# Performance work log

Measured on AMD Instinct MI355X. Metric: run time of the kernel, lower is better.

The kernel has to match this reference:

```python
import jax, jax.numpy as jnp
import numpy as np

L, H, DH = 2, 4, 64
D = H * DH                      # hidden_dim*heads = 256
B = 8                           # graphs per batch
NI_PG, ND_PG = 1024, 512        # inst/data nodes per graph
NI, ND = B * NI_PG, B * ND_PG
NPG = NI_PG + ND_PG
KPOOL = NPG // 2                # SAGPooling ratio=0.5
EC, EI, EO, EK = 65536, 32768, 32768, 8192


def setup_inputs():
    key = jax.random.key(0)
    ks = iter(jax.random.split(key, 64))
    def edges(ns, nd, e):
        k1, k2 = jax.random.split(next(ks))
        return jnp.stack([jax.random.randint(k1, (e,), 0, ns),
                          jax.random.randint(k2, (e,), 0, nd)]).astype(jnp.int32)
    inp = {}
    for g in ('g1', 'g2'):
        inp[g + '_x_inst'] = 0.1 * jax.random.normal(next(ks), (NI, D), jnp.float32)
        inp[g + '_x_data'] = 0.1 * jax.random.normal(next(ks), (ND, D), jnp.float32)
        inp[g + '_e_control'] = edges(NI, NI, EC)
        inp[g + '_e_input'] = edges(ND, NI, EI)
        inp[g + '_e_output'] = edges(NI, ND, EO)
        inp[g + '_e_call'] = edges(NI, NI, EK)
    s = 1.0 / np.sqrt(D)
    def w(*shape):
        return s * jax.random.normal(next(ks), shape, jnp.float32)
    for name in ('hgt_Wk', 'hgt_Wq', 'hgt_Wv', 'hgt_Wo'):
        inp[name] = w(L, 2, 2, D, D)   # [layer, direction, node_type, D, D]
    sh = 1.0 / np.sqrt(DH)
    inp['hgt_arel'] = sh * jax.random.normal(next(ks), (L, 2, 4, H, DH, DH), jnp.float32)
    inp['hgt_mrel'] = sh * jax.random.normal(next(ks), (L, 2, 4, H, DH, DH), jnp.float32)
    inp['hgt_prel'] = jnp.ones((L, 2, 4, H), jnp.float32)
    inp['hgt_skip'] = jnp.ones((L, 2, 2), jnp.float32)
    inp['pool_W'] = w(D, 1)
    inp['pool_att'] = 0.1 * jax.random.normal(next(ks), (2,), jnp.float32)
    inp['pool_bias'] = jnp.zeros((1,), jnp.float32)
    for name in ('trans_Wq', 'trans_Wk', 'trans_Wv', 'trans_Wo'):
        inp[name] = w(D, D)
    inp['trans_ln_g'] = jnp.ones((D,), jnp.float32)
    inp['trans_ln_b'] = jnp.zeros((D,), jnp.float32)
    return inp


def _seg_softmax_agg(scores, vals, col, n):
    # scores [E,H], vals [E,H,DH], softmax over incoming edges per dst node
    m = jax.ops.segment_max(scores, col, num_segments=n)
    a = jnp.exp(scores - m[col])
    den = jax.ops.segment_sum(a, col, num_segments=n)
    alpha = a / (den[col] + 1e-16)
    return jax.ops.segment_sum(alpha[..., None] * vals, col, num_segments=n)


def _hgt_conv(xs, rels, Wk, Wq, Wv, Wo, arel, mrel, prel, skip):
    # xs: [x_inst, x_data]; rels: list of (rel_idx, src_t, dst_t, row, col)
    ns = [x.shape[0] for x in xs]
    K = [(x @ Wk[t]).reshape(-1, H, DH) for t, x in enumerate(xs)]
    Q = [(x @ Wq[t]).reshape(-1, H, DH) for t, x in enumerate(xs)]
    V = [(x @ Wv[t]).reshape(-1, H, DH) for t, x in enumerate(xs)]
    buf = {0: ([], [], []), 1: ([], [], [])}
    for r, st, dt, row, col in rels:
        ke = jnp.einsum('ehd,hdf->ehf', K[st][row], arel[r])
        ve = jnp.einsum('ehd,hdf->ehf', V[st][row], mrel[r])
        sc = (Q[dt][col] * ke).sum(-1) * prel[r] / np.sqrt(DH)   # [E,H]
        buf[dt][0].append(sc); buf[dt][1].append(ve); buf[dt][2].append(col)
    out = []
    for t, x in enumerate(xs):
        sc = jnp.concatenate(buf[t][0])
        ve = jnp.concatenate(buf[t][1])
        col = jnp.concatenate(buf[t][2])
        agg = _seg_softmax_agg(sc, ve, col, ns[t]).reshape(ns[t], D)
        o = jax.nn.gelu(agg, approximate=False) @ Wo[t]
        g = jax.nn.sigmoid(skip[t])
        out.append(g * o + (1.0 - g) * x)
    return out


def _dir_hgt(xs, E, P, l):
    (rc, cc), (ri, ci), (ro, co), (rk, ck) = [(e[0], e[1]) for e in E]
    fwd_rels = [(0, 0, 0, rc, cc), (1, 1, 0, ri, ci), (2, 0, 1, ro, co), (3, 0, 0, rk, ck)]
    rev_rels = [(0, 0, 0, cc, rc), (1, 0, 1, ci, ri), (2, 1, 0, co, ro), (3, 0, 0, ck, rk)]
    of = _hgt_conv(xs, fwd_rels, *[p[l, 0] for p in P])
    orv = _hgt_conv(xs, rev_rels, *[p[l, 1] for p in P])
    return [0.5 * a + 0.5 * b for a, b in zip(of, orv)]   # alpha = 0.5


def _branch(x_i, x_d, ec, ei, eo, ek, P, pool_W, pool_att, pool_bias, tq, tk, tv, to, lg, lb):
    xs = [x_i, x_d]
    E = (ec, ei, eo, ek)
    for l in range(L):
        xs = _dir_hgt(xs, E, P, l)
        xs = [jax.nn.relu(x) for x in xs]        # dropout is identity at eval
    x = jnp.concatenate(xs, 0)                   # to_homogeneous: inst then data
    N = NI + ND
    loops = jnp.arange(N, dtype=jnp.int32)       # GATConv add_self_loops=True
    row = jnp.concatenate([ec[0], ei[0] + NI, eo[0], ek[0], loops])
    col = jnp.concatenate([ec[1], ei[1], eo[1] + NI, ek[1], loops])
    # SAGPooling score via 1-channel GATConv
    h = x @ pool_W                               # [N,1]
    e = jax.nn.leaky_relu(pool_att[0] * h[row, 0] + pool_att[1] * h[col, 0], negative_slope=0.2)
    m = jax.ops.segment_max(e, col, num_segments=N)
    a = jnp.exp(e - m[col])
    den = jax.ops.segment_sum(a, col, num_segments=N)
    score = jax.ops.segment_sum((a / (den[col] + 1e-16)) * h[row, 0], col, num_segments=N) + pool_bias[0]
    # regroup nodes per graph (graphs contiguous within each node type block)
    sg = jnp.concatenate([score[:NI].reshape(B, NI_PG), score[NI:].reshape(B, ND_PG)], 1)
    xg = jnp.concatenate([x[:NI].reshape(B, NI_PG, D), x[NI:].reshape(B, ND_PG, D)], 1)
    vals, idx = jax.lax.top_k(sg, KPOOL)
    xp = jnp.take_along_axis(xg, idx[:, :, None], axis=1) * jnp.tanh(vals)[:, :, None]
    # global transformer attention over pooled nodes of each graph (TransConv)
    q = (xp @ tq).reshape(B, KPOOL, H, DH)
    k_ = (xp @ tk).reshape(B, KPOOL, H, DH)
    v = (xp @ tv).reshape(B, KPOOL, H, DH)
    att = jax.nn.softmax(jnp.einsum('bqhd,bkhd->bhqk', q, k_) / np.sqrt(DH), -1)
    o = jnp.einsum('bhqk,bkhd->bqhd', att, v).reshape(B, KPOOL, D) @ to
    y = xp + o
    mu = y.mean(-1, keepdims=True)
    var = ((y - mu) ** 2).mean(-1, keepdims=True)
    gatt = lg * (y - mu) / jnp.sqrt(var + 1e-5) + lb
    feat = jnp.concatenate([xp, gatt], -1)       # [B, KPOOL, 2D]
    return feat.sum(1)                           # global_add_pool -> [B, 2D]


def reference(g1_x_inst, g1_x_data, g1_e_control, g1_e_input, g1_e_output, g1_e_call,
              g2_x_inst, g2_x_data, g2_e_control, g2_e_input, g2_e_output, g2_e_call,
              hgt_Wk, hgt_Wq, hgt_Wv, hgt_Wo, hgt_arel, hgt_mrel, hgt_prel, hgt_skip,
              pool_W, pool_att, pool_bias,
              trans_Wq, trans_Wk, trans_Wv, trans_Wo, trans_ln_g, trans_ln_b):
    P = (hgt_Wk, hgt_Wq, hgt_Wv, hgt_Wo, hgt_arel, hgt_mrel, hgt_prel, hgt_skip)
    u = _branch(g1_x_inst, g1_x_data, g1_e_control, g1_e_input, g1_e_output, g1_e_call,
                P, pool_W, pool_att, pool_bias, trans_Wq, trans_Wk, trans_Wv, trans_Wo,
                trans_ln_g, trans_ln_b)
    v = _branch(g2_x_inst, g2_x_data, g2_e_control, g2_e_input, g2_e_output, g2_e_call,
                P, pool_W, pool_att, pool_bias, trans_Wq, trans_Wk, trans_Wv, trans_Wo,
                trans_ln_g, trans_ln_b)
    num = (u * v).sum(-1)
    den = jnp.maximum(jnp.linalg.norm(u, axis=-1), 1e-8) * jnp.maximum(jnp.linalg.norm(v, axis=-1), 1e-8)
    return num / den                             # cosine similarity, [B]
```

## Files before the change

### kernel.cpp

```cpp
#include <hip/hip_runtime.h>
#include <math.h>
#include <stdint.h>

#define LL 2
#define HH 4
#define DHH 64
#define DD 256
#define BB 8
#define NI 8192
#define ND 4096
#define NROW 12288
#define KPOOL 768
#define EC 65536
#define EI 32768
#define EO 32768
#define EK 8192
#define EHGT (EC+EI+EO+EK)

typedef unsigned short u16;
typedef short bf16x8 __attribute__((ext_vector_type(8)));
typedef float f32x4 __attribute__((ext_vector_type(4)));
typedef unsigned short u16x4 __attribute__((ext_vector_type(4)));

__device__ inline float gelu_f(float x){ return 0.5f*x*(1.f+erff(x*0.70710678118654752f)); }
__device__ inline u16 f2b(float x){ uint32_t u=__float_as_uint(x); return (u16)((u + 0x7fffu + ((u>>16)&1u))>>16); }
__device__ inline float b2f(u16 h){ return __uint_as_float(((uint32_t)h)<<16); }

__global__ void fill_u32(uint32_t* p, uint32_t v, int n){
    int i = blockIdx.x*256 + threadIdx.x;
    if(i<n) p[i]=v;
}

__global__ void cvt_split(const float* __restrict__ A, int nA, const float* __restrict__ B, int nB,
                          u16* __restrict__ oh, u16* __restrict__ ol){
    int i = (blockIdx.x*256 + threadIdx.x)*4;
    int tot = nA + nB;
    if(i >= tot) return;
    float4 v = (i < nA) ? *(const float4*)(A + i) : *(const float4*)(B + (i - nA));
    float vv[4] = {v.x, v.y, v.z, v.w};
    u16x4 h4, l4;
    #pragma unroll
    for(int j=0;j<4;j++){
        float x = vv[j];
        u16 h = f2b(x);
        h4[j] = h;
        l4[j] = f2b(x - b2f(h));
    }
    *(u16x4*)(oh + i) = h4;
    *(u16x4*)(ol + i) = l4;
}

struct WCArgs { const float* in[8]; u16* oh[8]; u16* ol[8]; int cnt[8]; int nr; };
__global__ void wcvt_split(WCArgs a){
    int mat = blockIdx.y, ri = 0;
    while(ri < a.nr-1 && mat >= a.cnt[ri]){ mat -= a.cnt[ri]; ri++; }
    const float* in = a.in[ri] + (size_t)mat*65536;
    u16* oh = a.oh[ri] + (size_t)mat*65536;
    u16* ol = a.ol[ri] + (size_t)mat*65536;
    int n = blockIdx.x, k = threadIdx.x;
    float x = in[(size_t)k*DD + n];
    u16 h = f2b(x);
    oh[n*DD + k] = h;
    ol[n*DD + k] = f2b(x - b2f(h));
}

__global__ void wcvt_wo(const float* __restrict__ Wo, const float* __restrict__ skip,
                        u16* __restrict__ oh, u16* __restrict__ ol){
    int combo = blockIdx.y;
    int l = combo >> 1, t = combo & 1;
    int n = blockIdx.x, k = threadIdx.x;
    #pragma unroll
    for(int dir=0;dir<2;dir++){
        int wi = (l*2+dir)*2 + t;
        float gg = 1.f/(1.f+expf(-skip[wi]));
        float x = 0.5f*gg*Wo[(size_t)wi*65536 + (size_t)k*DD + n];
        size_t o = (size_t)combo*131072 + (size_t)n*512 + dir*256 + k;
        u16 hh = f2b(x);
        oh[o] = hh;
        ol[o] = f2b(x - b2f(hh));
    }
}

struct GDesc { const u16* Ah; const u16* Al; const u16* Bh; const u16* Bl;
               float* C; u16* Oh; u16* Ol;
               const float* X; const float* skipp;
               int mblks; int mode; int prec; int kdim; };
struct GArgs { GDesc d[20]; int nd; };

__global__ __launch_bounds__(256) void gemm_mfma(GArgs ga){
    __shared__ u16 SBUF[2*128*64];
    char* Abuf = (char*)SBUF;
    char* Bbuf = (char*)(SBUF + 128*64);
    int mb = blockIdx.x, di = 0;
    while(di < ga.nd-1 && mb >= ga.d[di].mblks){ mb -= ga.d[di].mblks; di++; }
    GDesc g = ga.d[di];
    const int prec = g.prec;
    const int KD = g.kdim;
    const int m0 = mb*128, n0 = blockIdx.y*128;
    const int tid = threadIdx.x;
    const int lane = tid & 63, wid = tid >> 6;
    const int wm = (wid>>1)*64, wn = (wid&1)*64;
    const int l15 = lane & 15, l4 = lane >> 4;
    const int srow = tid >> 1, hf = tid & 1;
    const int ssw = (srow&7)<<4;
    const int c0 = (hf*32) ^ ssw;
    const int c1 = (hf*32+16) ^ ssw;
    const int c2 = (64+hf*32) ^ ssw;
    const int c3 = (64+hf*32+16) ^ ssw;
    const int rbyte = srow*128;
    const u16* __restrict__ Aph = g.Ah + (size_t)(m0 + srow)*KD + hf*16;
    const u16* __restrict__ Apl = g.Al + (size_t)(m0 + srow)*KD + hf*16;
    const u16* __restrict__ Bph = g.Bh + (size_t)(n0 + srow)*KD + hf*16;
    const u16* __restrict__ Bpl = g.Bl + (size_t)(n0 + srow)*KD + hf*16;
    f32x4 acc[4][4] = {};
    bf16x8 r0, r1, r2, r3, r4, r5, r6, r7;
    r0 = *(const bf16x8*)(Aph);
    r1 = *(const bf16x8*)(Aph + 8);
    r4 = *(const bf16x8*)(Bph);
    r5 = *(const bf16x8*)(Bph + 8);
    if(!prec){
        r2 = *(const bf16x8*)(Apl);
        r3 = *(const bf16x8*)(Apl + 8);
        r6 = *(const bf16x8*)(Bpl);
        r7 = *(const bf16x8*)(Bpl + 8);
    }
    for(int k0=0;k0<KD;k0+=32){
        __syncthreads();
        *(bf16x8*)(Abuf + rbyte + c0) = r0; *(bf16x8*)(Abuf + rbyte + c1) = r1;
        *(bf16x8*)(Bbuf + rbyte + c0) = r4; *(bf16x8*)(Bbuf + rbyte + c1) = r5;
        if(!prec){
            *(bf16x8*)(Abuf + rbyte + c2) = r2; *(bf16x8*)(Abuf + rbyte + c3) = r3;
            *(bf16x8*)(Bbuf + rbyte + c2) = r6; *(bf16x8*)(Bbuf + rbyte + c3) = r7;
        }
        __syncthreads();
        if(k0 + 32 < KD){
            int kn = k0 + 32;
            r0 = *(const bf16x8*)(Aph + kn);     r1 = *(const bf16x8*)(Aph + kn + 8);
            r4 = *(const bf16x8*)(Bph + kn);     r5 = *(const bf16x8*)(Bph + kn + 8);
            if(!prec){
                r2 = *(const bf16x8*)(Apl + kn); r3 = *(const bf16x8*)(Apl + kn + 8);
                r6 = *(const bf16x8*)(Bpl + kn); r7 = *(const bf16x8*)(Bpl + kn + 8);
            }
        }
        bf16x8 afh[4], bfh[4];
        #pragma unroll
        for(int i=0;i<4;i++){
            int ar = wm + i*16 + l15;
            int abase = ar*128;
            afh[i] = *(const bf16x8*)(Abuf + abase + ((l4*16) ^ ((ar&7)<<4)));
            int br = wn + i*16 + l15;
            int bbase = br*128;
            bfh[i] = *(const bf16x8*)(Bbuf + bbase + ((l4*16) ^ ((br&7)<<4)));
        }
        #pragma unroll
        for(int i=0;i<4;i++)
            #pragma unroll
            for(int j=0;j<4;j++)
                acc[i][j] = __builtin_amdgcn_mfma_f32_16x16x32_bf16(afh[i], bfh[j], acc[i][j], 0,0,0);
        if(!prec){
            bf16x8 afl[4], bfl[4];
            #pragma unroll
            for(int i=0;i<4;i++){
                int ar = wm + i*16 + l15;
                int abase = ar*128;
                afl[i] = *(const bf16x8*)(Abuf + abase + ((64 + l4*16) ^ ((ar&7)<<4)));
                int br = wn + i*16 + l15;
                int bbase = br*128;
                bfl[i] = *(const bf16x8*)(Bbuf + bbase + ((64 + l4*16) ^ ((br&7)<<4)));
            }
            #pragma unroll
            for(int i=0;i<4;i++)
                #pragma unroll
                for(int j=0;j<4;j++){
                    acc[i][j] = __builtin_amdgcn_mfma_f32_16x16x32_bf16(afh[i], bfl[j], acc[i][j], 0,0,0);
                    acc[i][j] = __builtin_amdgcn_mfma_f32_16x16x32_bf16(afl[i], bfh[j], acc[i][j], 0,0,0);
                }
        }
    }
    const int mode = g.mode;
    float cx = 0.f;
    if(mode == 6){
        float g0 = 1.f/(1.f + expf(-g.skipp[0]));
        float g1 = 1.f/(1.f + expf(-g.skipp[2]));
        cx = 1.f - 0.5f*(g0 + g1);
    }
    float* LDSf = (float*)SBUF;
    const int lrow = tid >> 5;
    const int cc4 = (tid & 31)*4;
    #pragma unroll
    for(int half=0; half<2; half++){
        __syncthreads();
        if((wid>>1) == half){
            #pragma unroll
            for(int i=0;i<4;i++)
                #pragma unroll
                for(int j=0;j<4;j++)
                    #pragma unroll
                    for(int r=0;r<4;r++)
                        LDSf[(i*16 + l4*4 + r)*128 + wn + j*16 + l15] = acc[i][j][r];
        }
        __syncthreads();
        #pragma unroll
        for(int k=0;k<8;k++){
            int row = lrow + k*8;
            size_t o = (size_t)(m0 + half*64 + row)*DD + n0 + cc4;
            float4 v = *(const float4*)&LDSf[row*128 + cc4];
            float vv[4] = {v.x, v.y, v.z, v.w};
            if(mode==0){
                *(float4*)(g.C + o) = v;
            } else if(mode==4){
                u16x4 h4;
                #pragma unroll
                for(int j=0;j<4;j++) h4[j] = f2b(vv[j]);
                *(u16x4*)(g.Oh + o) = h4;
            } else {
                float4 x = *(const float4*)(g.X + o);
                float xx[4] = {x.x, x.y, x.z, x.w};
                float4 cv;
                float* cvv = (float*)&cv;
                u16x4 h4, lo4;
                #pragma unroll
                for(int j=0;j<4;j++){
                    float v3 = vv[j] + cx*xx[j];
                    v3 = v3 > 0.f ? v3 : 0.f;
                    cvv[j] = v3;
                    u16 hh = f2b(v3); h4[j]=hh; lo4[j]=f2b(v3-b2f(hh));
                }
                *(float4*)(g.C + o) = cv;
                *(u16x4*)(g.Oh + o) = h4;
                *(u16x4*)(g.Ol + o) = lo4;
            }
        }
    }
}

__global__ void combine_all(const float* __restrict__ Wk, const float* __restrict__ Wv,
                            const float* __restrict__ Ra, const float* __restrict__ Rm,
                            float* __restrict__ wtk, float* __restrict__ wtv){
    const int st_tab[2][4] = {{0,1,0,0},{0,0,1,0}};
    int combo = blockIdx.y;
    int idx = combo >> 1, kv = combo & 1;
    int r = idx & 3, wb = idx >> 2, dir = wb & 1;
    int st = st_tab[dir][r];
    const float* W = (kv ? Wv : Wk) + (size_t)(wb*2 + st)*65536;
    const float* R = (kv ? Rm : Ra) + (size_t)idx*16384;
    float* o = (kv ? wtv : wtk) + (size_t)idx*65536;
    int d = blockIdx.x, c = threadIdx.x;
    int h = c >> 6, f = c & 63;
    const float* Wrow = W + d*DD + h*64;
    const float* Rh = R + h*4096 + f;
    float s = 0.f;
    #pragma unroll 8
    for(int k=0;k<64;k++) s += Wrow[k]*Rh[k*64];
    o[d*DD + c] = s;
}

__device__ inline void edge_decode(int e, int& r, int& el){
    if(e < EC){ r=0; el=e; }
    else if(e < EC+EI){ r=1; el=e-EC; }
    else if(e < EC+EI+EO){ r=2; el=e-(EC+EI); }
    else { r=3; el=e-(EC+EI+EO); }
}

struct CB2 {
    const int* row[8]; const int* col[8];
    int dt[8]; int st[8];
    uint32_t* cnt; uint32_t* rowptr; uint32_t* einfo;
};

__global__ void csr_hist2(CB2 a){
    int ge = blockIdx.x*256 + threadIdx.x;
    if(ge >= 2*EHGT) return;
    int dir = ge >= EHGT;
    int e = ge - dir*EHGT;
    int r, el; edge_decode(e, r, el);
    int idx = dir*4 + r;
    int c = a.col[idx][el];
    int dst = dir*NROW + (a.dt[idx] ? (NI + c) : c);
    atomicAdd(&a.cnt[dst], 1u);
}

__global__ __launch_bounds__(1024) void scan_rowptr2(uint32_t* cnt, uint32_t* rowptr){
    __shared__ uint32_t part[1024];
    int t = threadIdx.x;
    int base = t*24;
    uint32_t lpre[24];
    uint32_t sum = 0;
    #pragma unroll
    for(int i=0;i<24;i++){
        uint32_t c = cnt[base+i];
        lpre[i] = sum; sum += c;
        cnt[base+i] = 0;
    }
    part[t] = sum;
    __syncthreads();
    for(int offs=1; offs<1024; offs<<=1){
        uint32_t v = (t>=offs) ? part[t-offs] : 0u;
        __syncthreads();
        part[t] += v;
        __syncthreads();
    }
    uint32_t pre = (t==0) ? 0u : part[t-1];
    #pragma unroll
    for(int i=0;i<24;i++) rowptr[base+i] = pre + lpre[i];
    if(t==1023) rowptr[2*NROW] = part[1023];
}

__global__ void csr_scatter2(CB2 a){
    int ge = blockIdx.x*256 + threadIdx.x;
    if(ge >= 2*EHGT) return;
    int dir = ge >= EHGT;
    int e = ge - dir*EHGT;
    int r, el; edge_decode(e, r, el);
    int idx = dir*4 + r;
    int c = a.col[idx][el];
    int dst = dir*NROW + (a.dt[idx] ? (NI + c) : c);
    int src = a.row[idx][el];
    uint32_t p = a.rowptr[dst] + atomicAdd(&a.cnt[dst], 1u);
    uint32_t vmidx = (uint32_t)(r*NI + src);
    uint32_t hom = a.st[idx] ? (uint32_t)(NI + src) : (uint32_t)src;
    a.einfo[p] = vmidx | (hom << 16);
}

__global__ __launch_bounds__(256) void hgt_fused(const uint32_t* __restrict__ rowptr,
                                                 const uint32_t* __restrict__ einfo,
                                                 const float* __restrict__ q_i,
                                                 const float* __restrict__ q_d,
                                                 const u16* __restrict__ ka,
                                                 const u16* __restrict__ vm,
                                                 const float* __restrict__ prel,
                                                 u16* __restrict__ bagg_h,
                                                 u16* __restrict__ bagg_l){
    int wv = threadIdx.x >> 6, lane = threadIdx.x & 63;
    int bx = blockIdx.x;
    int dir = bx >= (NROW/4);
    bx -= dir*(NROW/4);
    int rowi = bx*4 + wv;
    uint32_t p0 = rowptr[(size_t)dir*NROW + rowi], p1 = rowptr[(size_t)dir*NROW + rowi + 1];
    int h = lane >> 4;
    const float* qi = q_i + (size_t)dir*NI*DD;
    const float* qd = q_d + (size_t)dir*ND*DD;
    const u16* kad = ka + (size_t)dir*4*NI*DD;
    const u16* vmd = vm + (size_t)dir*4*NI*DD;
    const float* pr = prel + dir*4*HH;
    const float* qrow = (rowi < NI) ? (qi + (size_t)rowi*DD) : (qd + (size_t)(rowi-NI)*DD);
    float4 q4 = *(const float4*)(qrow + lane*4);
    float pr0 = pr[0*HH+h]*0.125f, pr1 = pr[1*HH+h]*0.125f;
    float pr2 = pr[2*HH+h]*0.125f, pr3 = pr[3*HH+h]*0.125f;
    float m = -INFINITY, den = 0.f;
    float4 o4 = {0.f,0.f,0.f,0.f};
    for(uint32_t p = p0; p < p1; p++){
        uint32_t vmidx = einfo[p] & 0xffffu;
        int r = vmidx >> 13;
        uint2 kr = *(const uint2*)(kad + (size_t)vmidx*DD + lane*4);
        uint2 vr = *(const uint2*)(vmd + (size_t)vmidx*DD + lane*4);
        float k0 = __uint_as_float(kr.x << 16), k1 = __uint_as_float(kr.x & 0xffff0000u);
        float k2 = __uint_as_float(kr.y << 16), k3 = __uint_as_float(kr.y & 0xffff0000u);
        float v0 = __uint_as_float(vr.x << 16), v1 = __uint_as_float(vr.x & 0xffff0000u);
        float v2 = __uint_as_float(vr.y << 16), v3 = __uint_as_float(vr.y & 0xffff0000u);
        float d = q4.x*k0 + q4.y*k1 + q4.z*k2 + q4.w*k3;
        d += __shfl_xor(d, 1); d += __shfl_xor(d, 2);
        d += __shfl_xor(d, 4); d += __shfl_xor(d, 8);
        float pf = (r==0) ? pr0 : (r==1) ? pr1 : (r==2) ? pr2 : pr3;
        float s = d * pf;
        float nm = fmaxf(m, s);
        float sc_ = expf(m - nm);
        float pe = expf(s - nm);
        den = den*sc_ + pe;
        o4.x = o4.x*sc_ + pe*v0;
        o4.y = o4.y*sc_ + pe*v1;
        o4.z = o4.z*sc_ + pe*v2;
        o4.w = o4.w*sc_ + pe*v3;
        m = nm;
    }
    float inv = 1.f/(den + 1e-16f);
    float vals[4] = {o4.x*inv, o4.y*inv, o4.z*inv, o4.w*inv};
    u16x4 h4, l4;
    #pragma unroll
    for(int j=0;j<4;j++){
        float g = gelu_f(vals[j]);
        u16 hh = f2b(g);
        h4[j] = hh;
        l4[j] = f2b(g - b2f(hh));
    }
    size_t ob = (size_t)rowi*512 + dir*256 + lane*4;
    *(u16x4*)(bagg_h + ob) = h4;
    *(u16x4*)(bagg_l + ob) = l4;
}

__global__ void pool_h2(const float* __restrict__ xi, const float* __restrict__ xd,
                        const float* __restrict__ w, float* __restrict__ h){
    int node = blockIdx.x*4 + (threadIdx.x>>6);
    int lane = threadIdx.x & 63;
    const float* xr = (node < NI) ? (xi + (size_t)node*DD) : (xd + (size_t)(node-NI)*DD);
    float s = 0.f;
    for(int j=lane;j<DD;j+=64) s += xr[j]*w[j];
    for(int m=32;m;m>>=1) s += __shfl_xor(s, m);
    if(lane==0) h[node] = s;
}

__global__ __launch_bounds__(256) void pool_csr(const uint32_t* __restrict__ rowptr,
                                                const uint32_t* __restrict__ einfo,
                                                const float* __restrict__ h,
                                                const float* __restrict__ att,
                                                float* __restrict__ score){
    int w = blockIdx.x*4 + (threadIdx.x >> 6);
    int lane = threadIdx.x & 63;
    if(w >= NROW) return;
    uint32_t p0 = rowptr[w], p1 = rowptr[w+1];
    float a0 = att[0], a1 = att[1];
    float hn = h[w];
    float es = a0*hn + a1*hn;
    es = es >= 0.f ? es : 0.2f*es;
    float m = -INFINITY;
    for(uint32_t p = p0+lane; p < p1; p += 64){
        float hs = h[einfo[p] >> 16];
        float e = a0*hs + a1*hn;
        e = e >= 0.f ? e : 0.2f*e;
        m = fmaxf(m, e);
    }
    #pragma unroll
    for(int s=32;s;s>>=1) m = fmaxf(m, __shfl_xor(m, s));
    m = fmaxf(m, es);
    float lden = 0.f, lnum = 0.f;
    for(uint32_t p = p0+lane; p < p1; p += 64){
        float hs = h[einfo[p] >> 16];
        float e = a0*hs + a1*hn;
        e = e >= 0.f ? e : 0.2f*e;
        float a = expf(e - m);
        lden += a; lnum += a*hs;
    }
    #pragma unroll
    for(int s=32;s;s>>=1){ lden += __shfl_xor(lden, s); lnum += __shfl_xor(lnum, s); }
    float aself = expf(es - m);
    lden += aself; lnum += aself*hn;
    if(lane==0) score[w] = lnum/(lden + 1e-16f);
}

__global__ __launch_bounds__(256) void topk_rank(const float* __restrict__ score,
                                                 const float* __restrict__ bias,
                                                 int* __restrict__ sel_node,
                                                 float* __restrict__ sel_scale){
    int b = blockIdx.y;
    int wid = threadIdx.x >> 6, lane = threadIdx.x & 63;
    int i = blockIdx.x*4 + wid;
    int nodei = (i<1024) ? (b*1024 + i) : (NI + b*512 + (i-1024));
    float ki = score[nodei];
    int r = 0;
    #pragma unroll
    for(int s=0;s<24;s++){
        int j = s*64 + lane;
        int nodej = (j<1024) ? (b*1024 + j) : (NI + b*512 + (j-1024));
        float kj = score[nodej];
        r += (kj > ki) || (kj == ki && j < i);
    }
    #pragma unroll
    for(int m=32;m;m>>=1) r += __shfl_xor(r, m);
    if(lane==0 && r < KPOOL){
        sel_node[b*KPOOL + r] = nodei;
        sel_scale[b*KPOOL + r] = tanhf(ki + bias[0]);
    }
}

__global__ void gather_xp(const int* __restrict__ sel, const float* __restrict__ scale,
                          const float* __restrict__ xi, const float* __restrict__ xd,
                          float* __restrict__ xp, u16* __restrict__ bh, u16* __restrict__ bl){
    int i = blockIdx.x*256 + threadIdx.x;
    int rowp = i >> 8, c = i & 255;
// ... 109 lines not shown
            size_t o = qrow*DD + h*64 + dhb*16 + l4*4 + r;
            u16 hh = f2b(val);
            aoh[o] = hh;
            aol[o] = f2b(val - b2f(hh));
        }
}

__global__ __launch_bounds__(256) void ln_kernel(const float* __restrict__ xp, const float* __restrict__ o2,
                                                 const float* __restrict__ lg, const float* __restrict__ lb,
                                                 float* __restrict__ gatt){
    __shared__ float red[256];
    int r = blockIdx.x, c = threadIdx.x;
    float y = xp[(size_t)r*DD + c] + o2[(size_t)r*DD + c];
    red[c] = y; __syncthreads();
    for(int s=128;s;s>>=1){ if(c<s) red[c] += red[c+s]; __syncthreads(); }
    float mu = red[0]*(1.f/DD);
    __syncthreads();
    float d = y - mu;
    red[c] = d*d; __syncthreads();
    for(int s=128;s;s>>=1){ if(c<s) red[c] += red[c+s]; __syncthreads(); }
    float var = red[0]*(1.f/DD);
    gatt[(size_t)r*DD + c] = lg[c]*d/sqrtf(var+1e-5f) + lb[c];
}

__global__ void feat_reduce2(const float* __restrict__ xp, const float* __restrict__ gatt,
                             float* __restrict__ out){
    int b = blockIdx.x, c = threadIdx.x;
    int j0 = blockIdx.y*64;
    float s1=0.f, s2=0.f;
    for(int j=j0;j<j0+64;j++){
        size_t base = ((size_t)(b*KPOOL + j))*DD + c;
        s1 += xp[base];
        s2 += gatt[base];
    }
    atomicAdd(&out[b*512 + c], s1);
    atomicAdd(&out[b*512 + 256 + c], s2);
}

__global__ void cosine_kernel(const float* __restrict__ u, const float* __restrict__ v,
                              float* __restrict__ out){
    int b = blockIdx.x, t = threadIdx.x;
    float du=0.f, nu=0.f, nv=0.f;
    for(int j=t;j<512;j+=64){
        float a = u[b*512+j], bb = v[b*512+j];
        du += a*bb; nu += a*a; nv += bb*bb;
    }
    for(int m=32;m;m>>=1){
        du += __shfl_xor(du,m); nu += __shfl_xor(nu,m); nv += __shfl_xor(nv,m);
    }
    if(t==0) out[b] = du / (fmaxf(sqrtf(nu),1e-8f)*fmaxf(sqrtf(nv),1e-8f));
}

extern "C" void kernel_launch(void* const* d_in, const int* in_sizes, int n_in,
                              void* d_out, int out_size, void* d_ws, size_t ws_size,
                              hipStream_t stream){
    (void)in_sizes; (void)n_in; (void)out_size; (void)ws_size;
    const float* hgt_Wk   = (const float*)d_in[12];
    const float* hgt_Wq   = (const float*)d_in[13];
    const float* hgt_Wv   = (const float*)d_in[14];
    const float* hgt_Wo   = (const float*)d_in[15];
    const float* hgt_arel = (const float*)d_in[16];
    const float* hgt_mrel = (const float*)d_in[17];
    const float* hgt_prel = (const float*)d_in[18];
    const float* hgt_skip = (const float*)d_in[19];
    const float* pool_W   = (const float*)d_in[20];
    const float* pool_att = (const float*)d_in[21];
    const float* pool_bias= (const float*)d_in[22];
    const float* t_wq     = (const float*)d_in[23];
    const float* t_wk     = (const float*)d_in[24];
    const float* t_wv     = (const float*)d_in[25];
    const float* t_wo     = (const float*)d_in[26];
    const float* ln_g     = (const float*)d_in[27];
    const float* ln_b     = (const float*)d_in[28];
    float* out = (float*)d_out;

    char* base = (char*)d_ws;
    size_t off = 0;
    auto allocb = [&](size_t nbytes)->void*{
        void* p = (void*)(base + off);
        off += ((nbytes + 255) & ~(size_t)255);
        return p;
    };
    const size_t MAT = 65536;
    u16* bwtk_h = (u16*)allocb(16*MAT*2); u16* bwtk_l = (u16*)allocb(16*MAT*2);
    u16* bwtv_h = (u16*)allocb(16*MAT*2); u16* bwtv_l = (u16*)allocb(16*MAT*2);
    u16* bwq_h  = (u16*)allocb(8*MAT*2);  u16* bwq_l  = (u16*)allocb(8*MAT*2);
    u16* bwoc_h = (u16*)allocb(4*131072*2); u16* bwoc_l = (u16*)allocb(4*131072*2);
    u16* btw_h  = (u16*)allocb(4*MAT*2);  u16* btw_l  = (u16*)allocb(4*MAT*2);
    float* ubuf = (float*)allocb(BB*512*4);
    float* vbuf = (float*)allocb(BB*512*4);
    float* xa_i = (float*)allocb((size_t)NI*DD*4);
    float* xa_d = (float*)allocb((size_t)ND*DD*4);
    float* xb_i = (float*)allocb((size_t)NI*DD*4);
    float* xb_d = (float*)allocb((size_t)ND*DD*4);
    uint32_t* ccnt   = (uint32_t*)allocb((size_t)2*NROW*4);
    uint32_t* rowptr = (uint32_t*)allocb((size_t)(2*NROW+1)*4);
    uint32_t* einfo  = (uint32_t*)allocb((size_t)2*EHGT*4);
    size_t region = off;
    float* q_i  = (float*)allocb((size_t)2*NI*DD*4);
    float* q_d  = (float*)allocb((size_t)2*ND*DD*4);
    u16* ka16 = (u16*)allocb((size_t)8*NI*DD*2);
    u16* vm16 = (u16*)allocb((size_t)8*NI*DD*2);
    u16* bcur_h = (u16*)allocb((size_t)NROW*DD*2);
    u16* bcur_l = (u16*)allocb((size_t)NROW*DD*2);
    u16* bagg_h = (u16*)allocb((size_t)NROW*512*2);
    u16* bagg_l = (u16*)allocb((size_t)NROW*512*2);
    off = region;
    float* hvec = (float*)allocb(NROW*4);
    float* pscore = (float*)allocb(NROW*4);
    int* seln   = (int*)allocb(BB*KPOOL*4);
    float* sels = (float*)allocb(BB*KPOOL*4);
    float* xp   = (float*)allocb((size_t)BB*KPOOL*DD*4);
    float* o2   = (float*)allocb((size_t)BB*KPOOL*DD*4);
    float* gatt = (float*)allocb((size_t)BB*KPOOL*DD*4);
    u16* bxp_h = (u16*)allocb((size_t)BB*KPOOL*DD*2);
    u16* bxp_l = (u16*)allocb((size_t)BB*KPOOL*DD*2);
    u16* qbh = (u16*)allocb((size_t)BB*KPOOL*DD*2);
    u16* kbh = (u16*)allocb((size_t)BB*KPOOL*DD*2);
    u16* vbh = (u16*)allocb((size_t)BB*KPOOL*DD*2);
    u16* bao_h = (u16*)allocb((size_t)BB*KPOOL*DD*2);
    u16* bao_l = (u16*)allocb((size_t)BB*KPOOL*DD*2);

    const int st_tab[2][4] = {{0,1,0,0},{0,0,1,0}};
    const int dt_tab[2][4] = {{0,0,1,0},{0,1,0,0}};
    const int MR = BB*KPOOL;

    fill_u32<<<(2*BB*512+255)/256,256,0,stream>>>((uint32_t*)ubuf, 0u, 2*BB*512);
    float* wtkF = (float*)ka16;
    float* wtvF = (float*)ka16 + 16*MAT;
    combine_all<<<dim3(256,32),256,0,stream>>>(hgt_Wk, hgt_Wv, hgt_arel, hgt_mrel, wtkF, wtvF);
    WCArgs wc;
    wc.in[0]=wtkF;   wc.oh[0]=bwtk_h; wc.ol[0]=bwtk_l; wc.cnt[0]=16;
    wc.in[1]=wtvF;   wc.oh[1]=bwtv_h; wc.ol[1]=bwtv_l; wc.cnt[1]=16;
    wc.in[2]=hgt_Wq; wc.oh[2]=bwq_h;  wc.ol[2]=bwq_l;  wc.cnt[2]=8;
    wc.in[3]=t_wq;   wc.oh[3]=btw_h;          wc.ol[3]=btw_l;          wc.cnt[3]=1;
    wc.in[4]=t_wk;   wc.oh[4]=btw_h+1*MAT;    wc.ol[4]=btw_l+1*MAT;    wc.cnt[4]=1;
    wc.in[5]=t_wv;   wc.oh[5]=btw_h+2*MAT;    wc.ol[5]=btw_l+2*MAT;    wc.cnt[5]=1;
    wc.in[6]=t_wo;   wc.oh[6]=btw_h+3*MAT;    wc.ol[6]=btw_l+3*MAT;    wc.cnt[6]=1;
    wc.nr = 7;
    wcvt_split<<<dim3(256,44),256,0,stream>>>(wc);
    wcvt_wo<<<dim3(256,4),256,0,stream>>>(hgt_Wo, hgt_skip, bwoc_h, bwoc_l);

    for(int bi=0;bi<2;bi++){
        int ib = bi*6;
        const float* x_inst = (const float*)d_in[ib+0];
        const float* x_data = (const float*)d_in[ib+1];
        const int* ecp = (const int*)d_in[ib+2];
        const int* eip = (const int*)d_in[ib+3];
        const int* eop = (const int*)d_in[ib+4];
        const int* ekp = (const int*)d_in[ib+5];
        const int* rows_f[4] = {ecp, eip, eop, ekp};
        const int* cols_f[4] = {ecp+EC, eip+EI, eop+EO, ekp+EK};

        CB2 cb;
        for(int r=0;r<4;r++){
            cb.row[r]   = rows_f[r]; cb.col[r]   = cols_f[r]; cb.dt[r]   = dt_tab[0][r]; cb.st[r]   = st_tab[0][r];
            cb.row[4+r] = cols_f[r]; cb.col[4+r] = rows_f[r]; cb.dt[4+r] = dt_tab[1][r]; cb.st[4+r] = st_tab[1][r];
        }
        cb.cnt = ccnt; cb.rowptr = rowptr; cb.einfo = einfo;
        fill_u32<<<(2*NROW+255)/256,256,0,stream>>>(ccnt, 0u, 2*NROW);
        csr_hist2<<<(2*EHGT+255)/256,256,0,stream>>>(cb);
        scan_rowptr2<<<1,1024,0,stream>>>(ccnt, rowptr);
        csr_scatter2<<<(2*EHGT+255)/256,256,0,stream>>>(cb);

        const float* cur_i = x_inst;
        const float* cur_d = x_data;
        cvt_split<<<((NROW*DD/4)+255)/256,256,0,stream>>>(cur_i, NI*DD, cur_d, ND*DD, bcur_h, bcur_l);
        for(int l=0;l<LL;l++){
            float* nxt_i = (l==0) ? xa_i : xb_i;
            float* nxt_d = (l==0) ? xa_d : xb_d;

            GArgs g1; int nb1 = 0, ndx = 0;
            auto addg = [&](int srctype, const u16* Bh, const u16* Bl, float* Cm, u16* Om, int M, int mode, int prec){
                GDesc& d = g1.d[ndx];
                size_t ao = srctype ? (size_t)NI*DD : 0;
                d.Ah = bcur_h + ao; d.Al = bcur_l + ao;
                d.Bh = Bh; d.Bl = Bl; d.C = Cm;
                d.Oh = Om; d.Ol = nullptr; d.X = nullptr; d.skipp = nullptr;
                d.mblks = M/128; d.mode = mode; d.prec = prec; d.kdim = 256;
                nb1 += M/128; ndx++;
            };
            for(int dir=0;dir<2;dir++){
                int wb = l*2 + dir;
                addg(0, bwq_h + (size_t)(wb*2+0)*MAT, bwq_l + (size_t)(wb*2+0)*MAT,
                     q_i + (size_t)dir*NI*DD, nullptr, NI, 0, 0);
                addg(1, bwq_h + (size_t)(wb*2+1)*MAT, bwq_l + (size_t)(wb*2+1)*MAT,
                     q_d + (size_t)dir*ND*DD, nullptr, ND, 0, 0);
                for(int r=0;r<4;r++){
                    int st = st_tab[dir][r];
                    addg(st, bwtk_h + (size_t)(wb*4+r)*MAT, bwtk_l + (size_t)(wb*4+r)*MAT,
                         nullptr, ka16 + (size_t)(dir*4 + r)*NI*DD, st ? ND : NI, 4, 1);
                }
                for(int r=0;r<4;r++){
                    int st = st_tab[dir][r];
                    addg(st, bwtv_h + (size_t)(wb*4+r)*MAT, bwtv_l + (size_t)(wb*4+r)*MAT,
                         nullptr, vm16 + (size_t)(dir*4 + r)*NI*DD, st ? ND : NI, 4, 1);
                }
            }
            g1.nd = ndx;
            gemm_mfma<<<dim3(nb1,2),256,0,stream>>>(g1);

            hgt_fused<<<2*(NROW/4),256,0,stream>>>(rowptr, einfo,
                q_i, q_d, ka16, vm16, hgt_prel + (size_t)l*2*4*HH, bagg_h, bagg_l);

            GArgs g3; g3.nd = 2;
            for(int t=0;t<2;t++){
                GDesc& d = g3.d[t];
                d.Ah = bagg_h + (t ? (size_t)NI*512 : 0);
                d.Al = bagg_l + (t ? (size_t)NI*512 : 0);
                d.Bh = bwoc_h + (size_t)(l*2+t)*131072;
                d.Bl = bwoc_l + (size_t)(l*2+t)*131072;
                d.C = t ? nxt_d : nxt_i;
                d.Oh = bcur_h + (t ? (size_t)NI*DD : 0);
                d.Ol = bcur_l + (t ? (size_t)NI*DD : 0);
                d.X = t ? cur_d : cur_i;
                d.skipp = hgt_skip + l*4 + t;
                d.mblks = (t ? ND : NI)/128;
                d.mode = 6; d.prec = 0; d.kdim = 512;
            }
            gemm_mfma<<<dim3(NI/128 + ND/128,2),256,0,stream>>>(g3);

            cur_i = nxt_i;
            cur_d = nxt_d;
        }

        pool_h2<<<NROW/4,256,0,stream>>>(cur_i, cur_d, pool_W, hvec);
        pool_csr<<<NROW/4,256,0,stream>>>(rowptr, einfo, hvec, pool_att, pscore);
        topk_rank<<<dim3(384,BB),256,0,stream>>>(pscore, pool_bias, seln, sels);
        gather_xp<<<BB*KPOOL,256,0,stream>>>(seln, sels, cur_i, cur_d, xp, bxp_h, bxp_l);

        GArgs g4; g4.nd = 3;
        for(int t=0;t<3;t++){
            GDesc& d = g4.d[t];
            d.Ah=bxp_h; d.Al=bxp_l;
            d.Bh=btw_h + (size_t)t*MAT; d.Bl=btw_l + (size_t)t*MAT;
            d.C = nullptr;
            d.Oh = (t==0)? qbh : (t==1)? kbh : vbh;
            d.Ol = nullptr;
            d.X = nullptr; d.skipp = nullptr;
            d.mblks = MR/128; d.mode = 4; d.prec = 0; d.kdim = 256;
        }
        gemm_mfma<<<dim3(3*(MR/128),2),256,0,stream>>>(g4);
        attn_mfma<<<dim3(BB*HH, KPOOL/64),256,0,stream>>>(qbh, kbh, vbh, bao_h, bao_l);
        GArgs g5; g5.nd = 1;
        {
            GDesc& d = g5.d[0];
            d.Ah=bao_h; d.Al=bao_l;
            d.Bh=btw_h + (size_t)3*MAT; d.Bl=btw_l + (size_t)3*MAT;
            d.C=o2; d.Oh=nullptr; d.Ol=nullptr; d.X=nullptr; d.skipp=nullptr;
            d.mblks=MR/128; d.mode=0; d.prec=0; d.kdim=256;
        }
        gemm_mfma<<<dim3(MR/128,2),256,0,stream>>>(g5);
        ln_kernel<<<MR,256,0,stream>>>(xp, o2, ln_g, ln_b, gatt);
        feat_reduce2<<<dim3(BB,12),256,0,stream>>>(xp, gatt, bi ? vbuf : ubuf);
    }

    cosine_kernel<<<BB,64,0,stream>>>(ubuf, vbuf, out);
}
```

Measured before the change: 917.9 us.

## Batch both graph branches into shared HGT GEMM and attention launches

Processes the two siamese branches together through the HGT layers. The GEMM kernels gain a blockIdx.z branch dimension with per-descriptor strides, and hgt_fused covers both branches per direction. Loop order is restructured so each direction runs its own projection GEMM and aggregation, with one output GEMM per layer covering both branches. The intent is to halve the number of launches and fill the GPU better, in exchange for doubled intermediate buffers (the projection and aggregation scratch regions grow) and a per-direction split of what used to be one projection launch.

```diff
diff --git a/kernel.cpp b/kernel.cpp
--- a/kernel.cpp
+++ b/kernel.cpp
@@ -32,7 +32,7 @@
 }
 
 __global__ void cvt_split(const float* __restrict__ A, int nA, const float* __restrict__ B, int nB,
-                          u16* __restrict__ oh, u16* __restrict__ ol){
+                          u16* __restrict__ oh, u16* __restrict__ ol, float* __restrict__ xc){
     int i = (blockIdx.x*256 + threadIdx.x)*4;
     int tot = nA + nB;
     if(i >= tot) return;
@@ -48,6 +48,7 @@
     }
     *(u16x4*)(oh + i) = h4;
     *(u16x4*)(ol + i) = l4;
+    *(float4*)(xc + i) = v;
 }
 
 struct WCArgs { const float* in[8]; u16* oh[8]; u16* ol[8]; int cnt[8]; int nr; };
@@ -84,6 +85,7 @@
 struct GDesc { const u16* Ah; const u16* Al; const u16* Bh; const u16* Bl;
                float* C; u16* Oh; u16* Ol;
                const float* X; const float* skipp;
+               size_t strA; size_t strC; size_t strO; size_t strX;
                int mblks; int mode; int prec; int kdim; };
 struct GArgs { GDesc d[20]; int nd; };
 
@@ -94,6 +96,9 @@
     int mb = blockIdx.x, di = 0;
     while(di < ga.nd-1 && mb >= ga.d[di].mblks){ mb -= ga.d[di].mblks; di++; }
     GDesc g = ga.d[di];
+    const size_t br = blockIdx.z;
+    const u16* gAh = g.Ah + br*g.strA;
+    const u16* gAl = g.Al + br*g.strA;
     const int prec = g.prec;
     const int KD = g.kdim;
     const int m0 = mb*128, n0 = blockIdx.y*128;
@@ -108,8 +113,8 @@
     const int c2 = (64+hf*32) ^ ssw;
     const int c3 = (64+hf*32+16) ^ ssw;
     const int rbyte = srow*128;
-    const u16* __restrict__ Aph = g.Ah + (size_t)(m0 + srow)*KD + hf*16;
-    const u16* __restrict__ Apl = g.Al + (size_t)(m0 + srow)*KD + hf*16;
+    const u16* __restrict__ Aph = gAh + (size_t)(m0 + srow)*KD + hf*16;
+    const u16* __restrict__ Apl = gAl + (size_t)(m0 + srow)*KD + hf*16;
     const u16* __restrict__ Bph = g.Bh + (size_t)(n0 + srow)*KD + hf*16;
     const u16* __restrict__ Bpl = g.Bl + (size_t)(n0 + srow)*KD + hf*16;
     f32x4 acc[4][4] = {};
@@ -148,9 +153,9 @@
             int ar = wm + i*16 + l15;
             int abase = ar*128;
             afh[i] = *(const bf16x8*)(Abuf + abase + ((l4*16) ^ ((ar&7)<<4)));
-            int br = wn + i*16 + l15;
-            int bbase = br*128;
-            bfh[i] = *(const bf16x8*)(Bbuf + bbase + ((l4*16) ^ ((br&7)<<4)));
+            int br_ = wn + i*16 + l15;
+            int bbase = br_*128;
+            bfh[i] = *(const bf16x8*)(Bbuf + bbase + ((l4*16) ^ ((br_&7)<<4)));
         }
         #pragma unroll
         for(int i=0;i<4;i++)
@@ -164,9 +169,9 @@
                 int ar = wm + i*16 + l15;
                 int abase = ar*128;
                 afl[i] = *(const bf16x8*)(Abuf + abase + ((64 + l4*16) ^ ((ar&7)<<4)));
-                int br = wn + i*16 + l15;
-                int bbase = br*128;
-                bfl[i] = *(const bf16x8*)(Bbuf + bbase + ((64 + l4*16) ^ ((br&7)<<4)));
+                int br_ = wn + i*16 + l15;
+                int bbase = br_*128;
+                bfl[i] = *(const bf16x8*)(Bbuf + bbase + ((64 + l4*16) ^ ((br_&7)<<4)));
             }
             #pragma unroll
             for(int i=0;i<4;i++)
@@ -178,6 +183,10 @@
         }
     }
     const int mode = g.mode;
+    float* Cb = g.C + br*g.strC;
+    u16* Ohb = g.Oh + br*g.strO;
+    u16* Olb = g.Ol + br*g.strO;
+    const float* Xb = g.X + br*g.strX;
     float cx = 0.f;
     if(mode == 6){
         float g0 = 1.f/(1.f + expf(-g.skipp[0]));
@@ -207,14 +216,14 @@
             float4 v = *(const float4*)&LDSf[row*128 + cc4];
             float vv[4] = {v.x, v.y, v.z, v.w};
             if(mode==0){
-                *(float4*)(g.C + o) = v;
+                *(float4*)(Cb + o) = v;
             } else if(mode==4){
                 u16x4 h4;
                 #pragma unroll
                 for(int j=0;j<4;j++) h4[j] = f2b(vv[j]);
-                *(u16x4*)(g.Oh + o) = h4;
+                *(u16x4*)(Ohb + o) = h4;
             } else {
-                float4 x = *(const float4*)(g.X + o);
+                float4 x = *(const float4*)(Xb + o);
                 float xx[4] = {x.x, x.y, x.z, x.w};
                 float4 cv;
                 float* cvv = (float*)&cv;
@@ -226,9 +235,9 @@
                     cvv[j] = v3;
                     u16 hh = f2b(v3); h4[j]=hh; lo4[j]=f2b(v3-b2f(hh));
                 }
-                *(float4*)(g.C + o) = cv;
-                *(u16x4*)(g.Oh + o) = h4;
-                *(u16x4*)(g.Ol + o) = lo4;
+                *(float4*)(Cb + o) = cv;
+                *(u16x4*)(Ohb + o) = h4;
+                *(u16x4*)(Olb + o) = lo4;
             }
         }
     }
@@ -330,27 +339,29 @@
                                                  const u16* __restrict__ vm,
                                                  const float* __restrict__ prel,
                                                  u16* __restrict__ bagg_h,
-                                                 u16* __restrict__ bagg_l){
+                                                 u16* __restrict__ bagg_l,
+                                                 int dir){
     int wv = threadIdx.x >> 6, lane = threadIdx.x & 63;
     int bx = blockIdx.x;
-    int dir = bx >= (NROW/4);
-    bx -= dir*(NROW/4);
+    int brx = 0;
+    if(bx >= (NROW/4)){ brx = 1; bx -= (NROW/4); }
     int rowi = bx*4 + wv;
-    uint32_t p0 = rowptr[(size_t)dir*NROW + rowi], p1 = rowptr[(size_t)dir*NROW + rowi + 1];
+    const uint32_t* rp = rowptr + (size_t)brx*(2*NROW+1) + (size_t)dir*NROW;
+    uint32_t p0 = rp[rowi], p1 = rp[rowi+1];
+    const uint32_t* ei = einfo + (size_t)brx*(2*EHGT);
     int h = lane >> 4;
-    const float* qi = q_i + (size_t)dir*NI*DD;
-    const float* qd = q_d + (size_t)dir*ND*DD;
-    const u16* kad = ka + (size_t)dir*4*NI*DD;
-    const u16* vmd = vm + (size_t)dir*4*NI*DD;
-    const float* pr = prel + dir*4*HH;
+    const float* qi = q_i + (size_t)brx*NI*DD;
+    const float* qd = q_d + (size_t)brx*ND*DD;
+    const u16* kad = ka + (size_t)brx*4*NI*DD;
+    const u16* vmd = vm + (size_t)brx*4*NI*DD;
     const float* qrow = (rowi < NI) ? (qi + (size_t)rowi*DD) : (qd + (size_t)(rowi-NI)*DD);
     float4 q4 = *(const float4*)(qrow + lane*4);
-    float pr0 = pr[0*HH+h]*0.125f, pr1 = pr[1*HH+h]*0.125f;
-    float pr2 = pr[2*HH+h]*0.125f, pr3 = pr[3*HH+h]*0.125f;
+    float pr0 = prel[0*HH+h]*0.125f, pr1 = prel[1*HH+h]*0.125f;
+    float pr2 = prel[2*HH+h]*0.125f, pr3 = prel[3*HH+h]*0.125f;
     float m = -INFINITY, den = 0.f;
     float4 o4 = {0.f,0.f,0.f,0.f};
     for(uint32_t p = p0; p < p1; p++){
-        uint32_t vmidx = einfo[p] & 0xffffu;
+        uint32_t vmidx = ei[p] & 0xffffu;
         int r = vmidx >> 13;
         uint2 kr = *(const uint2*)(kad + (size_t)vmidx*DD + lane*4);
         uint2 vr = *(const uint2*)(vmd + (size_t)vmidx*DD + lane*4);
@@ -383,7 +394,7 @@
         h4[j] = hh;
         l4[j] = f2b(g - b2f(hh));
     }
-    size_t ob = (size_t)rowi*512 + dir*256 + lane*4;
+    size_t ob = (size_t)brx*NROW*512 + (size_t)rowi*512 + dir*256 + lane*4;
     *(u16x4*)(bagg_h + ob) = h4;
     *(u16x4*)(bagg_l + ob) = l4;
 }
@@ -659,6 +670,7 @@
         return p;
     };
     const size_t MAT = 65536;
+    const size_t BRN = (size_t)NROW*DD;
     u16* bwtk_h = (u16*)allocb(16*MAT*2); u16* bwtk_l = (u16*)allocb(16*MAT*2);
     u16* bwtv_h = (u16*)allocb(16*MAT*2); u16* bwtv_l = (u16*)allocb(16*MAT*2);
     u16* bwq_h  = (u16*)allocb(8*MAT*2);  u16* bwq_l  = (u16*)allocb(8*MAT*2);
@@ -666,22 +678,20 @@
     u16* btw_h  = (u16*)allocb(4*MAT*2);  u16* btw_l  = (u16*)allocb(4*MAT*2);
     float* ubuf = (float*)allocb(BB*512*4);
     float* vbuf = (float*)allocb(BB*512*4);
-    float* xa_i = (float*)allocb((size_t)NI*DD*4);
-    float* xa_d = (float*)allocb((size_t)ND*DD*4);
-    float* xb_i = (float*)allocb((size_t)NI*DD*4);
-    float* xb_d = (float*)allocb((size_t)ND*DD*4);
+    float* xa   = (float*)allocb(2*BRN*4);
+    float* xcur = (float*)allocb(2*BRN*4);
     uint32_t* ccnt   = (uint32_t*)allocb((size_t)2*NROW*4);
-    uint32_t* rowptr = (uint32_t*)allocb((size_t)(2*NROW+1)*4);
-    uint32_t* einfo  = (uint32_t*)allocb((size_t)2*EHGT*4);
+    uint32_t* rowptr = (uint32_t*)allocb((size_t)2*(2*NROW+1)*4);
+    uint32_t* einfo  = (uint32_t*)allocb((size_t)2*2*EHGT*4);
     size_t region = off;
     float* q_i  = (float*)allocb((size_t)2*NI*DD*4);
     float* q_d  = (float*)allocb((size_t)2*ND*DD*4);
     u16* ka16 = (u16*)allocb((size_t)8*NI*DD*2);
     u16* vm16 = (u16*)allocb((size_t)8*NI*DD*2);
-    u16* bcur_h = (u16*)allocb((size_t)NROW*DD*2);
-    u16* bcur_l = (u16*)allocb((size_t)NROW*DD*2);
-    u16* bagg_h = (u16*)allocb((size_t)NROW*512*2);
-    u16* bagg_l = (u16*)allocb((size_t)NROW*512*2);
+    u16* bcur_h = (u16*)allocb(2*BRN*2);
+    u16* bcur_l = (u16*)allocb(2*BRN*2);
+    u16* bagg_h = (u16*)allocb((size_t)2*NROW*512*2);
+    u16* bagg_l = (u16*)allocb((size_t)2*NROW*512*2);
     off = region;
     float* hvec = (float*)allocb(NROW*4);
     float* pscore = (float*)allocb(NROW*4);
@@ -728,81 +738,89 @@
         const int* ekp = (const int*)d_in[ib+5];
         const int* rows_f[4] = {ecp, eip, eop, ekp};
         const int* cols_f[4] = {ecp+EC, eip+EI, eop+EO, ekp+EK};
-
         CB2 cb;
         for(int r=0;r<4;r++){
             cb.row[r]   = rows_f[r]; cb.col[r]   = cols_f[r]; cb.dt[r]   = dt_tab[0][r]; cb.st[r]   = st_tab[0][r];
             cb.row[4+r] = cols_f[r]; cb.col[4+r] = rows_f[r]; cb.dt[4+r] = dt_tab[1][r]; cb.st[4+r] = st_tab[1][r];
         }
-        cb.cnt = ccnt; cb.rowptr = rowptr; cb.einfo = einfo;
+        cb.cnt = ccnt;
+        cb.rowptr = rowptr + (size_t)bi*(2*NROW+1);
+        cb.einfo = einfo + (size_t)bi*(2*EHGT);
         fill_u32<<<(2*NROW+255)/256,256,0,stream>>>(ccnt, 0u, 2*NROW);
         csr_hist2<<<(2*EHGT+255)/256,256,0,stream>>>(cb);
-        scan_rowptr2<<<1,1024,0,stream>>>(ccnt, rowptr);
+        scan_rowptr2<<<1,1024,0,stream>>>(ccnt, cb.rowptr);
         csr_scatter2<<<(2*EHGT+255)/256,256,0,stream>>>(cb);
-
-        const float* cur_i = x_inst;
-        const float* cur_d = x_data;
-        cvt_split<<<((NROW*DD/4)+255)/256,256,0,stream>>>(cur_i, NI*DD, cur_d, ND*DD, bcur_h, bcur_l);
-        for(int l=0;l<LL;l++){
-            float* nxt_i = (l==0) ? xa_i : xb_i;
-            float* nxt_d = (l==0) ? xa_d : xb_d;
-
+        cvt_split<<<((NROW*DD/4)+255)/256,256,0,stream>>>(x_inst, NI*DD, x_data, ND*DD,
+            bcur_h + bi*BRN, bcur_l + bi*BRN, xcur + bi*BRN);
+    }
+
+    for(int l=0;l<LL;l++){
+        float* curX = (l==0) ? xcur : xa;
+        float* nxtX = (l==0) ? xa : xcur;
+
+        for(int dir=0;dir<2;dir++){
+            int wb = l*2 + dir;
             GArgs g1; int nb1 = 0, ndx = 0;
-            auto addg = [&](int srctype, const u16* Bh, const u16* Bl, float* Cm, u16* Om, int M, int mode, int prec){
+            auto addg = [&](int srctype, const u16* Bh, const u16* Bl, float* Cm, u16* Om,
+                            size_t strC, size_t strO, int M, int mode, int prec){
                 GDesc& d = g1.d[ndx];
                 size_t ao = srctype ? (size_t)NI*DD : 0;
                 d.Ah = bcur_h + ao; d.Al = bcur_l + ao;
                 d.Bh = Bh; d.Bl = Bl; d.C = Cm;
                 d.Oh = Om; d.Ol = nullptr; d.X = nullptr; d.skipp = nullptr;
+                d.strA = BRN; d.strC = strC; d.strO = strO; d.strX = 0;
                 d.mblks = M/128; d.mode = mode; d.prec = prec; d.kdim = 256;
                 nb1 += M/128; ndx++;
             };
-            for(int dir=0;dir<2;dir++){
-                int wb = l*2 + dir;
-                addg(0, bwq_h + (size_t)(wb*2+0)*MAT, bwq_l + (size_t)(wb*2+0)*MAT,
-                     q_i + (size_t)dir*NI*DD, nullptr, NI, 0, 0);
-                addg(1, bwq_h + (size_t)(wb*2+1)*MAT, bwq_l + (size_t)(wb*2+1)*MAT,
-                     q_d + (size_t)dir*ND*DD, nullptr, ND, 0, 0);
-                for(int r=0;r<4;r++){
-                    int st = st_tab[dir][r];
-                    addg(st, bwtk_h + (size_t)(wb*4+r)*MAT, bwtk_l + (size_t)(wb*4+r)*MAT,
-                         nullptr, ka16 + (size_t)(dir*4 + r)*NI*DD, st ? ND : NI, 4, 1);
-                }
-                for(int r=0;r<4;r++){
-                    int st = st_tab[dir][r];
-                    addg(st, bwtv_h + (size_t)(wb*4+r)*MAT, bwtv_l + (size_t)(wb*4+r)*MAT,
-                         nullptr, vm16 + (size_t)(dir*4 + r)*NI*DD, st ? ND : NI, 4, 1);
-                }
+            addg(0, bwq_h + (size_t)(wb*2+0)*MAT, bwq_l + (size_t)(wb*2+0)*MAT,
+                 q_i, nullptr, (size_t)NI*DD, 0, NI, 0, 0);
+            addg(1, bwq_h + (size_t)(wb*2+1)*MAT, bwq_l + (size_t)(wb*2+1)*MAT,
+                 q_d, nullptr, (size_t)ND*DD, 0, ND, 0, 0);
+            for(int r=0;r<4;r++){
+                int st = st_tab[dir][r];
+                addg(st, bwtk_h + (size_t)(wb*4+r)*MAT, bwtk_l + (size_t)(wb*4+r)*MAT,
+                     nullptr, ka16 + (size_t)r*NI*DD, 0, (size_t)4*NI*DD, st ? ND : NI, 4, 1);
+            }
+            for(int r=0;r<4;r++){
+                int st = st_tab[dir][r];
+                addg(st, bwtv_h + (size_t)(wb*4+r)*MAT, bwtv_l + (size_t)(wb*4+r)*MAT,
+                     nullptr, vm16 + (size_t)r*NI*DD, 0, (size_t)4*NI*DD, st ? ND : NI, 4, 1);
             }
             g1.nd = ndx;
-            gemm_mfma<<<dim3(nb1,2),256,0,stream>>>(g1);
+            gemm_mfma<<<dim3(nb1,2,2),256,0,stream>>>(g1);
 
             hgt_fused<<<2*(NROW/4),256,0,stream>>>(rowptr, einfo,
-                q_i, q_d, ka16, vm16, hgt_prel + (size_t)l*2*4*HH, bagg_h, bagg_l);
-
-            GArgs g3; g3.nd = 2;
-            for(int t=0;t<2;t++){
-                GDesc& d = g3.d[t];
-                d.Ah = bagg_h + (t ? (size_t)NI*512 : 0);
-                d.Al = bagg_l + (t ? (size_t)NI*512 : 0);
-                d.Bh = bwoc_h + (size_t)(l*2+t)*131072;
-                d.Bl = bwoc_l + (size_t)(l*2+t)*131072;
-                d.C = t ? nxt_d : nxt_i;
-                d.Oh = bcur_h + (t ? (size_t)NI*DD : 0);
-                d.Ol = bcur_l + (t ? (size_t)NI*DD : 0);
-                d.X = t ? cur_d : cur_i;
-                d.skipp = hgt_skip + l*4 + t;
-                d.mblks = (t ? ND : NI)/128;
-                d.mode = 6; d.prec = 0; d.kdim = 512;
-            }
-            gemm_mfma<<<dim3(NI/128 + ND/128,2),256,0,stream>>>(g3);
-
-            cur_i = nxt_i;
-            cur_d = nxt_d;
-        }
+                q_i, q_d, ka16, vm16, hgt_prel + (size_t)wb*4*HH, bagg_h, bagg_l, dir);
+        }
+
+        GArgs g3; g3.nd = 2;
+        for(int t=0;t<2;t++){
+            GDesc& d = g3.d[t];
+            size_t ao = t ? (size_t)NI*DD : 0;
+            d.Ah = bagg_h + (t ? (size_t)NI*512 : 0);
+            d.Al = bagg_l + (t ? (size_t)NI*512 : 0);
+            d.Bh = bwoc_h + (size_t)(l*2+t)*131072;
+            d.Bl = bwoc_l + (size_t)(l*2+t)*131072;
+            d.C = nxtX + ao;
+            d.Oh = bcur_h + ao;
+            d.Ol = bcur_l + ao;
+            d.X = curX + ao;
+            d.skipp = hgt_skip + l*4 + t;
+            d.strA = (size_t)NROW*512; d.strC = BRN; d.strO = BRN; d.strX = BRN;
+            d.mblks = (t ? ND : NI)/128;
+            d.mode = 6; d.prec = 0; d.kdim = 512;
+        }
+        gemm_mfma<<<dim3(NI/128 + ND/128,2,2),256,0,stream>>>(g3);
+    }
+
+    for(int bi=0;bi<2;bi++){
+        const float* cur_i = xcur + (size_t)bi*BRN;
+        const float* cur_d = cur_i + (size_t)NI*DD;
+        const uint32_t* rp = rowptr + (size_t)bi*(2*NROW+1);
+        const uint32_t* ei = einfo + (size_t)bi*(2*EHGT);
 
         pool_h2<<<NROW/4,256,0,stream>>>(cur_i, cur_d, pool_W, hvec);
-        pool_csr<<<NROW/4,256,0,stream>>>(rowptr, einfo, hvec, pool_att, pscore);
+        pool_csr<<<NROW/4,256,0,stream>>>(rp, ei, hvec, pool_att, pscore);
         topk_rank<<<dim3(384,BB),256,0,stream>>>(pscore, pool_bias, seln, sels);
         gather_xp<<<BB*KPOOL,256,0,stream>>>(seln, sels, cur_i, cur_d, xp, bxp_h, bxp_l);
 
@@ -815,9 +833,10 @@
             d.Oh = (t==0)? qbh : (t==1)? kbh : vbh;
             d.Ol = nullptr;
             d.X = nullptr; d.skipp = nullptr;
+            d.strA=0; d.strC=0; d.strO=0; d.strX=0;
             d.mblks = MR/128; d.mode = 4; d.prec = 0; d.kdim = 256;
         }
-        gemm_mfma<<<dim3(3*(MR/128),2),256,0,stream>>>(g4);
+        gemm_mfma<<<dim3(3*(MR/128),2,1),256,0,stream>>>(g4);
         attn_mfma<<<dim3(BB*HH, KPOOL/64),256,0,stream>>>(qbh, kbh, vbh, bao_h, bao_l);
         GArgs g5; g5.nd = 1;
         {
@@ -825,9 +844,10 @@
             d.Ah=bao_h; d.Al=bao_l;
             d.Bh=btw_h + (size_t)3*MAT; d.Bl=btw_l + (size_t)3*MAT;
             d.C=o2; d.Oh=nullptr; d.Ol=nullptr; d.X=nullptr; d.skipp=nullptr;
+            d.strA=0; d.strC=0; d.strO=0; d.strX=0;
             d.mblks=MR/128; d.mode=0; d.prec=0; d.kdim=256;
         }
-        gemm_mfma<<<dim3(MR/128,2),256,0,stream>>>(g5);
+        gemm_mfma<<<dim3(MR/128,2,1),256,0,stream>>>(g5);
         ln_kernel<<<MR,256,0,stream>>>(xp, o2, ln_g, ln_b, gatt);
         feat_reduce2<<<dim3(BB,12),256,0,stream>>>(xp, gatt, bi ? vbuf : ubuf);
     }
```

Measured after the change: 888.9 us. 1.03x faster.
